# Kernel tuning notes

Hardware: AMD Instinct MI355X
Metric: run time of the kernel (lower is better)

Reference implementation:

```python
import jax, jax.numpy as jnp
import numpy as np

N = 20000        # nodes per type
E = 320000       # edges per type (avg degree 16)
H = 8            # heads
F0 = 128         # initial feature dim
F_UNI = 256      # n_unified
F_OUT = 64       # n_units per layer
N_USER = 20000   # shape_ret[0]
N_CLASSES = 2


def setup_inputs() -> dict:
    key = jax.random.key(0)
    ks = jax.random.split(key, 32)
    nrm = lambda k, s: jax.random.normal(k, s, dtype=jnp.float32) * 0.05
    inp = {
        "hemb0": nrm(ks[0], (N, F0)),
        "hemb1": nrm(ks[1], (N, F0)),
        "W0": nrm(ks[2], (F0, F_UNI)),
        "W1": nrm(ks[3], (F0, F_UNI)),
    }
    i = 4
    for t in range(2):
        for l, fin in enumerate([F_UNI, H * F_OUT]):
            inp[f"g{t}l{l}_w"] = nrm(ks[i], (H, fin, F_OUT)); i += 1
            inp[f"g{t}l{l}_asrc"] = nrm(ks[i], (H, F_OUT)); i += 1
            inp[f"g{t}l{l}_atrg"] = nrm(ks[i], (H, F_OUT)); i += 1
    inp["aw1"] = nrm(ks[i], (F_UNI, F_OUT)); i += 1
    inp["aw2"] = nrm(ks[i], (F_OUT, F_OUT)); i += 1
    inp["am"] = nrm(ks[i], (F_OUT,)); i += 1
    inp["fc_w"] = nrm(ks[i], (F_OUT * 3, N_CLASSES)); i += 1
    inp["fc_b"] = jnp.zeros((N_CLASSES,), jnp.float32); i += 1
    inp["edge0"] = jax.random.randint(ks[i], (2, E), 0, N, dtype=jnp.int32); i += 1
    inp["edge1"] = jax.random.randint(ks[i], (2, E), 0, N, dtype=jnp.int32)
    return inp


def spgat(h, src, trg, w, asrc, atrg):
    """Sparse GAT layer: h [N,f_in], edge list src/trg [E] -> [N,H,f_out]."""
    n = h.shape[0]
    hp = jnp.einsum('nf,hfo->hno', h, w)              # [H,N,O]
    s = jnp.einsum('hno,ho->nh', hp, asrc)            # [N,H]
    t = jnp.einsum('hno,ho->nh', hp, atrg)            # [N,H]
    e = jax.nn.leaky_relu(s[src] + t[trg], negative_slope=0.2)  # [E,H]
    ex = jnp.exp(e - jnp.max(e))                      # global max shift (as in source)
    denom = jax.ops.segment_sum(ex, trg, num_segments=n)[trg] + 1e-16
    alpha = ex / denom                                # [E,H]
    msg = jnp.transpose(hp, (1, 0, 2))[src] * alpha[:, :, None]  # [E,H,O]
    return jax.ops.segment_sum(msg, trg, num_segments=n)         # [N,H,O]


def reference(hemb0, hemb1, W0, W1,
              g0l0_w, g0l0_asrc, g0l0_atrg, g0l1_w, g0l1_asrc, g0l1_atrg,
              g1l0_w, g1l0_asrc, g1l0_atrg, g1l1_w, g1l1_asrc, g1l1_atrg,
              aw1, aw2, am, fc_w, fc_b, edge0, edge1):
    trans0 = hemb0 @ W0                                # [N,F_UNI]
    trans1 = hemb1 @ W1
    stacks = [
        (trans0, edge0, (g0l0_w, g0l0_asrc, g0l0_atrg), (g0l1_w, g0l1_asrc, g0l1_atrg)),
        (trans1, edge1, (g1l0_w, g1l0_asrc, g1l0_atrg), (g1l1_w, g1l1_asrc, g1l1_atrg)),
    ]
    heter = []
    for trans, edge, p0, p1 in stacks:
        src, trg = edge[0], edge[1]
        x = spgat(trans, src, trg, *p0)                # [N,H,F_OUT]
        x = jax.nn.elu(x.reshape(N, -1))               # [N,H*F_OUT]
        x = spgat(x, src, trg, *p1).mean(axis=1)       # [N,F_OUT]
        heter.append(x[:N_USER][:, None, :])
    type_aware = jnp.concatenate(heter, axis=1)        # [N_USER, 2, F_OUT]
    # faithful to source: feature = trans_emb[0] where trans_emb is the LAST
    # type's transformed embedding -> row 0, shape [F_UNI], broadcast over nodes
    feature = trans1[0]
    q = jnp.tanh(feature @ aw1 + type_aware @ aw2)     # [N_USER,2,F_OUT]
    beta = jax.nn.softmax(q @ am, axis=-1)             # [N_USER,2]
    fusion = jnp.einsum('nr,nrd->nd', beta, type_aware)[:, None, :]
    ret = jnp.concatenate([type_aware, fusion], axis=1).reshape(N_USER, -1)
    return jax.nn.log_softmax(ret @ fc_w + fc_b, axis=-1)   # [N_USER, 2]
```

## Files before the change

kernel.cpp:

```cpp
#include <hip/hip_runtime.h>
#include <hip/hip_bf16.h>


typedef __hip_bfloat16 bf16;
typedef __attribute__((ext_vector_type(8))) short short8;
typedef __attribute__((ext_vector_type(4))) float f32x4;

__device__ __forceinline__ float bf2f(bf16 v) { return __bfloat162float(v); }
__device__ __forceinline__ float ldin(const void* p, long i, int f32) {
  return f32 ? ((const float*)p)[i] : bf2f(((const bf16*)p)[i]);
}
__device__ __forceinline__ short f2bfbits(float f) {
  bf16 h = __float2bfloat16(f);
  return *reinterpret_cast<short*>(&h);
}
__device__ __forceinline__ float bfbits2f(short b) {
  unsigned u = ((unsigned)(unsigned short)b) << 16;
  return __uint_as_float(u);
}

__global__ __launch_bounds__(64) void detect_kernel(const void* __restrict__ x,
                                                    int* __restrict__ flag) {
  int tid = threadIdx.x;
  float m = 0.f;
  for (int i = tid; i < 2048; i += 64) {
    float v = fabsf(bf2f(((const bf16*)x)[i]));
    if (!(v <= 1e3f)) v = 1e9f;
    m = fmaxf(m, v);
  }
#pragma unroll
  for (int off = 32; off; off >>= 1) m = fmaxf(m, __shfl_xor(m, off));
  if (tid == 0) flag[0] = (m > 1e3f) ? 1 : 0;
}

#define GBM 128
#define GBN 64
#define GBK 64

__device__ __forceinline__ int swz(int row, int kbyte) {
  return row * 128 + (kbyte ^ ((row & 7) << 4));
}

__global__ __launch_bounds__(256) void gemm_mfma(const void* __restrict__ A, int amode,
                                                 const void* __restrict__ B, int bmode,
                                                 bf16* __restrict__ C,
                                                 int M, int K, int Nc,
                                                 const void* __restrict__ stasrc,
                                                 const void* __restrict__ statrg,
                                                 float* __restrict__ svp,
                                                 float* __restrict__ tvp,
                                                 const int* __restrict__ flag) {
  __shared__ bf16 As[GBM * GBK];
  __shared__ bf16 Bs[GBN * GBK];
  const int f32 = flag[0];
  const int af32 = (amode == 1) ? f32 : 0;
  const int m0 = blockIdx.x * GBM;
  const int n0 = blockIdx.y * GBN;
  const int tid = threadIdx.x;
  const int lane = tid & 63;
  const int wrow = (tid >> 6) * 32;

  f32x4 acc[2][4];
#pragma unroll
  for (int m = 0; m < 2; m++)
#pragma unroll
    for (int n = 0; n < 4; n++)
#pragma unroll
      for (int r = 0; r < 4; r++) acc[m][n][r] = 0.f;

  for (int kt = 0; kt < K; kt += GBK) {
#pragma unroll
    for (int j = 0; j < 4; j++) {
      int idx = tid + j * 256;
      int row = idx >> 3;
      int ks = idx & 7;
      int gm = m0 + row;
      short8 v;
#pragma unroll
      for (int e = 0; e < 8; e++) v[e] = 0;
      if (gm < M) {
        long base = (long)gm * K + kt + ks * 8;
        if (!af32) {
          v = *(const short8*)((const bf16*)A + base);
        } else {
          const float* Af = (const float*)A + base;
#pragma unroll
          for (int e = 0; e < 8; e++) v[e] = f2bfbits(Af[e]);
        }
      }
      *(short8*)((char*)As + swz(row, ks * 16)) = v;
    }
    {
      int n = tid & 63;
      int ks0 = tid >> 6;
#pragma unroll
      for (int jj = 0; jj < 2; jj++) {
        int ks = ks0 + jj * 4;
        int k = kt + ks * 8;
        int col = n0 + n;
        long base;
        int cstr;
        if (bmode == 0) { base = (long)k * Nc + col; cstr = Nc; }
        else { base = ((long)(col >> 6) * K + k) * 64 + (col & 63); cstr = 64; }
        short8 v;
        if (f32) {
          const float* Bf = (const float*)B;
#pragma unroll
          for (int e = 0; e < 8; e++) v[e] = f2bfbits(Bf[base + (long)e * cstr]);
        } else {
          const bf16* Bh = (const bf16*)B;
#pragma unroll
          for (int e = 0; e < 8; e++) v[e] = *(const short*)&Bh[base + (long)e * cstr];
        }
        *(short8*)((char*)Bs + swz(n, ks * 16)) = v;
      }
    }
    __syncthreads();
#pragma unroll
    for (int kh = 0; kh < 2; kh++) {
      int klane = kh * 64 + ((lane >> 4) << 4);
      short8 af[2], bfr[4];
#pragma unroll
      for (int m = 0; m < 2; m++) {
        int row = wrow + m * 16 + (lane & 15);
        af[m] = *(const short8*)((const char*)As + swz(row, klane));
      }
#pragma unroll
      for (int n = 0; n < 4; n++) {
        int col = n * 16 + (lane & 15);
        bfr[n] = *(const short8*)((const char*)Bs + swz(col, klane));
      }
#pragma unroll
      for (int m = 0; m < 2; m++)
#pragma unroll
        for (int n = 0; n < 4; n++)
          acc[m][n] = __builtin_amdgcn_mfma_f32_16x16x32_bf16(af[m], bfr[n], acc[m][n], 0, 0, 0);
    }
    __syncthreads();
  }
  if (svp) {
    const int h = blockIdx.y;
    const int cl = lane & 15;
    float av[4], bv[4];
#pragma unroll
    for (int n = 0; n < 4; n++) {
      av[n] = ldin(stasrc, h * 64 + n * 16 + cl, f32);
      bv[n] = ldin(statrg, h * 64 + n * 16 + cl, f32);
    }
#pragma unroll
    for (int m = 0; m < 2; m++) {
#pragma unroll
      for (int r = 0; r < 4; r++) {
        float s = 0.f, t = 0.f;
#pragma unroll
        for (int n = 0; n < 4; n++) {
          s += acc[m][n][r] * av[n];
          t += acc[m][n][r] * bv[n];
        }
#pragma unroll
        for (int off = 1; off <= 8; off <<= 1) {
          s += __shfl_xor(s, off);
          t += __shfl_xor(t, off);
        }
        int row = m0 + wrow + m * 16 + ((lane >> 4) << 2) + r;
        if (cl == 0 && row < M) {
          svp[(long)row * 8 + h] = s;
          tvp[(long)row * 8 + h] = t;
        }
      }
    }
  }
#pragma unroll
  for (int m = 0; m < 2; m++) {
#pragma unroll
    for (int r = 0; r < 4; r++) {
      int row = m0 + wrow + m * 16 + ((lane >> 4) << 2) + r;
      if (row < M) {
#pragma unroll
        for (int n = 0; n < 4; n++) {
          int col = n0 + n * 16 + (lane & 15);
          C[(long)row * Nc + col] = __float2bfloat16(acc[m][n][r]);
        }
      }
    }
  }
}

__global__ void hist_kernel(const int* __restrict__ trg, int* __restrict__ deg, int E) {
  int e = blockIdx.x * 256 + threadIdx.x;
  if (e < E) atomicAdd(&deg[trg[e]], 1);
}

__global__ __launch_bounds__(1024) void scan_kernel(const int* __restrict__ deg,
                                                    int* __restrict__ row_ptr,
                                                    int* __restrict__ fil, int N) {
  __shared__ int sums[1024];
  int tid = threadIdx.x;
  int chunk = (N + 1023) >> 10;
  int start = tid * chunk;
  int end = start + chunk;
  if (start > N) start = N;
  if (end > N) end = N;
  int s = 0;
  for (int i = start; i < end; i++) s += deg[i];
  sums[tid] = s;
  __syncthreads();
  for (int off = 1; off < 1024; off <<= 1) {
    int add = (tid >= off) ? sums[tid - off] : 0;
    __syncthreads();
    sums[tid] += add;
    __syncthreads();
  }
  int run = (tid > 0) ? sums[tid - 1] : 0;
  for (int i = start; i < end; i++) {
    row_ptr[i] = run;
    fil[i] = run;
    run += deg[i];
  }
  if (tid == 0) row_ptr[N] = sums[1023];
}

__global__ void fill_kernel(const int* __restrict__ src, const int* __restrict__ trg,
                            int* __restrict__ fil, int* __restrict__ col, int E) {
  int e = blockIdx.x * 256 + threadIdx.x;
  if (e >= E) return;
  int t = trg[e];
  int pos = atomicAdd(&fil[t], 1);
  col[pos] = src[e];
}

__device__ __forceinline__ float exleaky(float v) {
  v = v > 0.f ? v : 0.2f * v;
  return __expf(v);
}

__global__ __launch_bounds__(256) void aggregate(const bf16* __restrict__ hp,
                                                 const float* __restrict__ sv,
                                                 const float* __restrict__ tv,
                                                 const int* __restrict__ row_ptr,
                                                 const int* __restrict__ col_src,
                                                 void* __restrict__ out, int N, int mode) {
  const int wid = threadIdx.x >> 6;
  const int lane = threadIdx.x & 63;
  const int n = blockIdx.x * 4 + wid;
  if (n >= N) return;
  const int start = row_ptr[n];
  const int deg = row_ptr[n + 1] - start;
  const int h = lane >> 3;
  const float tvh = tv[(long)n * 8 + h];
  const bf16* __restrict__ hpc = hp + lane * 8;

  float acc[8] = {0.f, 0.f, 0.f, 0.f, 0.f, 0.f, 0.f, 0.f};
  float den = 1e-16f;

#define AG_LOAD(E, V0, V1, V2, V3, Q0, Q1, Q2, Q3)                  \
  {                                                                 \
    int t0 = __shfl(mysrc, (E) + 0), t1 = __shfl(mysrc, (E) + 1);   \
    int t2 = __shfl(mysrc, (E) + 2), t3 = __shfl(mysrc, (E) + 3);   \
    V0 = *(const short8*)(hpc + (long)t0 * 512);                    \
    V1 = *(const short8*)(hpc + (long)t1 * 512);                    \
    V2 = *(const short8*)(hpc + (long)t2 * 512);                    \
    V3 = *(const short8*)(hpc + (long)t3 * 512);                    \
    Q0 = sv[(long)t0 * 8 + h];                                      \
    Q1 = sv[(long)t1 * 8 + h];                                      \
    Q2 = sv[(long)t2 * 8 + h];                                      \
    Q3 = sv[(long)t3 * 8 + h];                                      \
  }
#define AG_ACC(V0, V1, V2, V3, Q0, Q1, Q2, Q3)                      \
  {                                                                 \
    float a0 = exleaky(Q0 + tvh), a1 = exleaky(Q1 + tvh);           \
    float a2 = exleaky(Q2 + tvh), a3 = exleaky(Q3 + tvh);           \
    den += a0 + a1 + a2 + a3;                                       \
    _Pragma("unroll")                                               \
    for (int j = 0; j < 8; j++)                                     \
      acc[j] += a0 * bfbits2f(V0[j]) + a1 * bfbits2f(V1[j]) +       \
                a2 * bfbits2f(V2[j]) + a3 * bfbits2f(V3[j]);        \
  }

  for (int base = 0; base < deg; base += 64) {
    int cnt = deg - base;
    if (cnt > 64) cnt = 64;
    int mysrc = (lane < cnt) ? col_src[start + base + lane] : 0;
    int nfull = cnt & ~3;
    if (nfull) {
      short8 v0, v1, v2, v3;
      float q0, q1, q2, q3;
      AG_LOAD(0, v0, v1, v2, v3, q0, q1, q2, q3);
      for (int e = 4; e < nfull; e += 4) {
        short8 w0 = v0, w1 = v1, w2 = v2, w3 = v3;
        float p0 = q0, p1 = q1, p2 = q2, p3 = q3;
        AG_LOAD(e, v0, v1, v2, v3, q0, q1, q2, q3);
        AG_ACC(w0, w1, w2, w3, p0, p1, p2, p3);
      }
      AG_ACC(v0, v1, v2, v3, q0, q1, q2, q3);
    }
    for (int e = nfull; e < cnt; e++) {
      int s0 = __shfl(mysrc, e);
      short8 v = *(const short8*)(hpc + (long)s0 * 512);
      float a = exleaky(sv[(long)s0 * 8 + h] + tvh);
      den += a;
#pragma unroll
      for (int j = 0; j < 8; j++) acc[j] += a * bfbits2f(v[j]);
    }
  }

  const float dinv = 1.f / den;
  if (mode == 0) {
    short8 o8;
#pragma unroll
    for (int j = 0; j < 8; j++) {
      float s = acc[j] * dinv;
      float ev = s > 0.f ? s : expm1f(s);
      o8[j] = f2bfbits(ev);
    }
    *(short8*)((bf16*)out + (long)n * 512 + lane * 8) = o8;
  } else {
    float r[8];
#pragma unroll
    for (int j = 0; j < 8; j++) r[j] = acc[j] * dinv;
#pragma unroll
    for (int m = 8; m <= 32; m <<= 1)
#pragma unroll
      for (int j = 0; j < 8; j++) r[j] += __shfl_xor(r[j], m);
    if (lane < 8) {
      float* o = (float*)out + (long)n * 128 + lane * 8;
#pragma unroll
      for (int j = 0; j < 8; j++) o[j] = r[j] * 0.125f;
    }
  }
}

__global__ __launch_bounds__(64) void favec_kernel(const bf16* __restrict__ trans1,
                                                   const void* __restrict__ aw1,
                                                   float* __restrict__ favec,
                                                   const int* __restrict__ flag) {
  const int f32 = flag[0];
  int o = threadIdx.x;
  float acc = 0.f;
  for (int k = 0; k < 256; k++) acc += bf2f(trans1[k]) * ldin(aw1, k * 64 + o, f32);
  favec[o] = acc;
}

__global__ __launch_bounds__(64) void final_kernel(const float* __restrict__ ta,
                                                   const float* __restrict__ favec,
                                                   const void* __restrict__ aw2,
                                                   const void* __restrict__ am,
                                                   const void* __restrict__ fcw,
                                                   const void* __restrict__ fcb,
                                                   void* __restrict__ out, int N,
                                                   const int* __restrict__ flag) {
  const int f32 = flag[0];
  int n = blockIdx.x;
  int o = threadIdx.x;
  __shared__ float s0[64], s1[64];
  float ta0 = ta[(long)n * 128 + o];
  float ta1 = ta[(long)n * 128 + 64 + o];
  s0[o] = ta0;
  s1[o] = ta1;
  __syncthreads();
  float f = favec[o];
  float acc0 = f, acc1 = f;
  for (int k = 0; k < 64; k++) {
    float w = ldin(aw2, k * 64 + o, f32);
    acc0 += s0[k] * w;
    acc1 += s1[k] * w;
  }
  float amv = ldin(am, o, f32);
  float p0 = tanhf(acc0) * amv;
  float p1 = tanhf(acc1) * amv;
#pragma unroll
  for (int off = 32; off > 0; off >>= 1) {
    p0 += __shfl_xor(p0, off);
    p1 += __shfl_xor(p1, off);
  }
  float mx = fmaxf(p0, p1);
  float e0 = __expf(p0 - mx), e1 = __expf(p1 - mx);
  float b0 = e0 / (e0 + e1), b1 = e1 / (e0 + e1);
  float fus = b0 * ta0 + b1 * ta1;
  float l0 = ta0 * ldin(fcw, o * 2 + 0, f32) + ta1 * ldin(fcw, (64 + o) * 2 + 0, f32) +
             fus * ldin(fcw, (128 + o) * 2 + 0, f32);
  float l1 = ta0 * ldin(fcw, o * 2 + 1, f32) + ta1 * ldin(fcw, (64 + o) * 2 + 1, f32) +
             fus * ldin(fcw, (128 + o) * 2 + 1, f32);
#pragma unroll
  for (int off = 32; off > 0; off >>= 1) {
    l0 += __shfl_xor(l0, off);
    l1 += __shfl_xor(l1, off);
  }
  if (o == 0) {
    l0 += ldin(fcb, 0, f32);
    l1 += ldin(fcb, 1, f32);
    float m2 = fmaxf(l0, l1);
    float lse = m2 + logf(__expf(l0 - m2) + __expf(l1 - m2));
    if (f32) {
      ((float*)out)[n * 2 + 0] = l0 - lse;
      ((float*)out)[n * 2 + 1] = l1 - lse;
    } else {
      ((bf16*)out)[n * 2 + 0] = __float2bfloat16(l0 - lse);
      ((bf16*)out)[n * 2 + 1] = __float2bfloat16(l1 - lse);
    }
  }
}

extern "C" void kernel_launch(void* const* d_in, const int* in_sizes, int n_in,
                              void* d_out, int out_size, void* d_ws, size_t ws_size,
                              hipStream_t stream) {
  constexpr int N = 20000, E = 320000, H = 8, F0 = 128, FU = 256, FO = 64;
  const void* hemb[2] = {d_in[0], d_in[1]};
  const void* W[2] = {d_in[2], d_in[3]};
  const void* gw[2][2] = {{d_in[4], d_in[7]}, {d_in[10], d_in[13]}};
  const void* gasrc[2][2] = {{d_in[5], d_in[8]}, {d_in[11], d_in[14]}};
  const void* gatrg[2][2] = {{d_in[6], d_in[9]}, {d_in[12], d_in[15]}};
  const void* aw1 = d_in[16];
  const void* aw2 = d_in[17];
  const void* am = d_in[18];
  const void* fcw = d_in[19];
  const void* fcb = d_in[20];
  const int* edge[2] = {(const int*)d_in[21], (const int*)d_in[22]};

  char* p = (char*)d_ws;
  auto alloc = [&](size_t bytes) -> void* {
    void* r = (void*)p;
    p += (bytes + 255) & ~(size_t)255;
    return r;
  };
  int* flag = (int*)alloc(4);
  bf16* trans = (bf16*)alloc((size_t)N * FU * 2);
  bf16* hp = (bf16*)alloc((size_t)N * H * FO * 2);
  bf16* xbuf = (bf16*)alloc((size_t)N * H * FO * 2);
  float* sv = (float*)alloc((size_t)N * H * 4);
  float* tv = (float*)alloc((size_t)N * H * 4);
  float* ta = (float*)alloc((size_t)N * 2 * FO * 4);
  float* favec = (float*)alloc(FO * 4);
  int* deg[2];
  int* rp[2];
  int* fil[2];
  int* col[2];
  for (int t = 0; t < 2; t++) {
    deg[t] = (int*)alloc((size_t)N * 4);
    rp[t] = (int*)alloc((size_t)(N + 1) * 4);
    fil[t] = (int*)alloc((size_t)N * 4);
    col[t] = (int*)alloc((size_t)E * 4);
  }

  detect_kernel<<<1, 64, 0, stream>>>(hemb[0], flag);

  for (int t = 0; t < 2; t++) {
    hipMemsetAsync(deg[t], 0, (size_t)N * 4, stream);
    hist_kernel<<<(E + 255) / 256, 256, 0, stream>>>(edge[t] + E, deg[t], E);
    scan_kernel<<<1, 1024, 0, stream>>>(deg[t], rp[t], fil[t], N);
    fill_kernel<<<(E + 255) / 256, 256, 0, stream>>>(edge[t], edge[t] + E, fil[t], col[t], E);
  }

  const int gmx = (N + GBM - 1) / GBM;
  const int gagg = (N + 3) / 4;

  for (int t = 0; t < 2; t++) {
    gemm_mfma<<<dim3(gmx, FU / GBN), 256, 0, stream>>>(hemb[t], 1, W[t], 0, trans,
                                                       N, F0, FU,
                                                       nullptr, nullptr, nullptr, nullptr, flag);
    gemm_mfma<<<dim3(gmx, (H * FO) / GBN), 256, 0, stream>>>(trans, 0, gw[t][0], 1, hp,
                                                             N, FU, H * FO,
                                                             gasrc[t][0], gatrg[t][0], sv, tv, flag);
    aggregate<<<gagg, 256, 0, stream>>>(hp, sv, tv, rp[t], col[t], xbuf, N, 0);
    gemm_mfma<<<dim3(gmx, (H * FO) / GBN), 256, 0, stream>>>(xbuf, 0, gw[t][1], 1, hp,
                                                             N, H * FO, H * FO,
                                                             gasrc[t][1], gatrg[t][1], sv, tv, flag);
    aggregate<<<gagg, 256, 0, stream>>>(hp, sv, tv, rp[t], col[t], ta + t * FO, N, 1);
  }

  favec_kernel<<<1, 64, 0, stream>>>(trans, aw1, favec, flag);
  final_kernel<<<N, 64, 0, stream>>>(ta, favec, aw2, am, fcw, fcb, d_out, N, flag);
}
```

Baseline: 626.5 us.

## Split node aggregation across two waves, batch CSR build, tile final kernel

The aggregate kernel now assigns two wavefronts per destination node, each handling alternating groups of four edges, and combines their partial sums through shared memory. The goal is more memory-level parallelism for the gather-heavy aggregation. The CSR construction for both edge types is merged into single histogram, scan and fill launches to cut launch count. The final kernel processes four nodes per block, with weights staged in shared memory and activations broadcast by shuffles instead of per-node global reloads. The price is a block-wide sync and extra shared memory in aggregate, which may reduce occupancy.

```diff
diff --git a/kernel.cpp b/kernel.cpp
--- a/kernel.cpp
+++ b/kernel.cpp
@@ -186,14 +186,19 @@
   }
 }
 
-__global__ void hist_kernel(const int* __restrict__ trg, int* __restrict__ deg, int E) {
+__global__ void hist2_kernel(const int* __restrict__ trg0, const int* __restrict__ trg1,
+                             int* __restrict__ deg, int E, int N) {
   int e = blockIdx.x * 256 + threadIdx.x;
-  if (e < E) atomicAdd(&deg[trg[e]], 1);
-}
-
-__global__ __launch_bounds__(1024) void scan_kernel(const int* __restrict__ deg,
-                                                    int* __restrict__ row_ptr,
-                                                    int* __restrict__ fil, int N) {
+  if (e < E) atomicAdd(&deg[trg0[e]], 1);
+  else if (e < 2 * E) atomicAdd(&deg[N + trg1[e - E]], 1);
+}
+
+__global__ __launch_bounds__(1024) void scan_kernel(const int* __restrict__ degb,
+                                                    int* __restrict__ rpb,
+                                                    int* __restrict__ filb, int N) {
+  const int* deg = degb + (long)blockIdx.x * N;
+  int* row_ptr = rpb + (long)blockIdx.x * (N + 1);
+  int* fil = filb + (long)blockIdx.x * N;
   __shared__ int sums[1024];
   int tid = threadIdx.x;
   int chunk = (N + 1023) >> 10;
@@ -220,13 +225,20 @@
   if (tid == 0) row_ptr[N] = sums[1023];
 }
 
-__global__ void fill_kernel(const int* __restrict__ src, const int* __restrict__ trg,
-                            int* __restrict__ fil, int* __restrict__ col, int E) {
+__global__ void fill2_kernel(const int* __restrict__ src0, const int* __restrict__ trg0,
+                             const int* __restrict__ src1, const int* __restrict__ trg1,
+                             int* __restrict__ filb, int* __restrict__ colb, int E, int N) {
   int e = blockIdx.x * 256 + threadIdx.x;
-  if (e >= E) return;
-  int t = trg[e];
-  int pos = atomicAdd(&fil[t], 1);
-  col[pos] = src[e];
+  if (e < E) {
+    int t = trg0[e];
+    int pos = atomicAdd(&filb[t], 1);
+    colb[pos] = src0[e];
+  } else if (e < 2 * E) {
+    int ee = e - E;
+    int t = trg1[ee];
+    int pos = atomicAdd(&filb[N + t], 1);
+    colb[E + pos] = src1[ee];
+  }
 }
 
 __device__ __forceinline__ float exleaky(float v) {
@@ -240,23 +252,30 @@
                                                  const int* __restrict__ row_ptr,
                                                  const int* __restrict__ col_src,
                                                  void* __restrict__ out, int N, int mode) {
+  __shared__ float s_acc[2][512];
+  __shared__ float s_den[2][64];
   const int wid = threadIdx.x >> 6;
   const int lane = threadIdx.x & 63;
-  const int n = blockIdx.x * 4 + wid;
-  if (n >= N) return;
-  const int start = row_ptr[n];
-  const int deg = row_ptr[n + 1] - start;
+  const int slot = wid >> 1;
+  const int half = wid & 1;
+  const int n = blockIdx.x * 2 + slot;
+  const int act = (n < N);
+  int start = 0, deg = 0;
+  if (act) {
+    start = row_ptr[n];
+    deg = row_ptr[n + 1] - start;
+  }
   const int h = lane >> 3;
-  const float tvh = tv[(long)n * 8 + h];
+  const float tvh = act ? tv[(long)n * 8 + h] : 0.f;
   const bf16* __restrict__ hpc = hp + lane * 8;
 
   float acc[8] = {0.f, 0.f, 0.f, 0.f, 0.f, 0.f, 0.f, 0.f};
-  float den = 1e-16f;
-
-#define AG_LOAD(E, V0, V1, V2, V3, Q0, Q1, Q2, Q3)                  \
+  float den = 0.f;
+
+#define AG_LOAD(EB, V0, V1, V2, V3, Q0, Q1, Q2, Q3)                 \
   {                                                                 \
-    int t0 = __shfl(mysrc, (E) + 0), t1 = __shfl(mysrc, (E) + 1);   \
-    int t2 = __shfl(mysrc, (E) + 2), t3 = __shfl(mysrc, (E) + 3);   \
+    int t0 = __shfl(mysrc, (EB) + 0), t1 = __shfl(mysrc, (EB) + 1); \
+    int t2 = __shfl(mysrc, (EB) + 2), t3 = __shfl(mysrc, (EB) + 3); \
     V0 = *(const short8*)(hpc + (long)t0 * 512);                    \
     V1 = *(const short8*)(hpc + (long)t1 * 512);                    \
     V2 = *(const short8*)(hpc + (long)t2 * 512);                    \
@@ -281,51 +300,65 @@
     int cnt = deg - base;
     if (cnt > 64) cnt = 64;
     int mysrc = (lane < cnt) ? col_src[start + base + lane] : 0;
-    int nfull = cnt & ~3;
-    if (nfull) {
+    int ngrp = cnt >> 2;
+    int g = half;
+    if (g < ngrp) {
       short8 v0, v1, v2, v3;
       float q0, q1, q2, q3;
-      AG_LOAD(0, v0, v1, v2, v3, q0, q1, q2, q3);
-      for (int e = 4; e < nfull; e += 4) {
+      AG_LOAD(g * 4, v0, v1, v2, v3, q0, q1, q2, q3);
+      for (int g2 = g + 2; g2 < ngrp; g2 += 2) {
         short8 w0 = v0, w1 = v1, w2 = v2, w3 = v3;
         float p0 = q0, p1 = q1, p2 = q2, p3 = q3;
-        AG_LOAD(e, v0, v1, v2, v3, q0, q1, q2, q3);
+        AG_LOAD(g2 * 4, v0, v1, v2, v3, q0, q1, q2, q3);
         AG_ACC(w0, w1, w2, w3, p0, p1, p2, p3);
       }
       AG_ACC(v0, v1, v2, v3, q0, q1, q2, q3);
     }
-    for (int e = nfull; e < cnt; e++) {
-      int s0 = __shfl(mysrc, e);
-      short8 v = *(const short8*)(hpc + (long)s0 * 512);
-      float a = exleaky(sv[(long)s0 * 8 + h] + tvh);
-      den += a;
-#pragma unroll
-      for (int j = 0; j < 8; j++) acc[j] += a * bfbits2f(v[j]);
-    }
-  }
-
-  const float dinv = 1.f / den;
-  if (mode == 0) {
-    short8 o8;
-#pragma unroll
-    for (int j = 0; j < 8; j++) {
-      float s = acc[j] * dinv;
-      float ev = s > 0.f ? s : expm1f(s);
-      o8[j] = f2bfbits(ev);
-    }
-    *(short8*)((bf16*)out + (long)n * 512 + lane * 8) = o8;
-  } else {
-    float r[8];
-#pragma unroll
-    for (int j = 0; j < 8; j++) r[j] = acc[j] * dinv;
-#pragma unroll
-    for (int m = 8; m <= 32; m <<= 1)
-#pragma unroll
-      for (int j = 0; j < 8; j++) r[j] += __shfl_xor(r[j], m);
-    if (lane < 8) {
-      float* o = (float*)out + (long)n * 128 + lane * 8;
-#pragma unroll
-      for (int j = 0; j < 8; j++) o[j] = r[j] * 0.125f;
+    if (half == 0) {
+      for (int e = ngrp * 4; e < cnt; e++) {
+        int s0 = __shfl(mysrc, e);
+        short8 v = *(const short8*)(hpc + (long)s0 * 512);
+        float a = exleaky(sv[(long)s0 * 8 + h] + tvh);
+        den += a;
+#pragma unroll
+        for (int j = 0; j < 8; j++) acc[j] += a * bfbits2f(v[j]);
+      }
+    }
+  }
+
+  if (half == 1) {
+#pragma unroll
+    for (int j = 0; j < 8; j++) s_acc[slot][j * 64 + lane] = acc[j];
+    s_den[slot][lane] = den;
+  }
+  __syncthreads();
+  if (half == 0 && act) {
+    den += s_den[slot][lane] + 1e-16f;
+#pragma unroll
+    for (int j = 0; j < 8; j++) acc[j] += s_acc[slot][j * 64 + lane];
+    const float dinv = 1.f / den;
+    if (mode == 0) {
+      short8 o8;
+#pragma unroll
+      for (int j = 0; j < 8; j++) {
+        float s = acc[j] * dinv;
+        float ev = s > 0.f ? s : expm1f(s);
+        o8[j] = f2bfbits(ev);
+      }
+      *(short8*)((bf16*)out + (long)n * 512 + lane * 8) = o8;
+    } else {
+      float r[8];
+#pragma unroll
+      for (int j = 0; j < 8; j++) r[j] = acc[j] * dinv;
+#pragma unroll
+      for (int m = 8; m <= 32; m <<= 1)
+#pragma unroll
+        for (int j = 0; j < 8; j++) r[j] += __shfl_xor(r[j], m);
+      if (lane < 8) {
+        float* o = (float*)out + (long)n * 128 + lane * 8;
+#pragma unroll
+        for (int j = 0; j < 8; j++) o[j] = r[j] * 0.125f;
+      }
     }
   }
 }
@@ -341,31 +374,37 @@
   favec[o] = acc;
 }
 
-__global__ __launch_bounds__(64) void final_kernel(const float* __restrict__ ta,
-                                                   const float* __restrict__ favec,
-                                                   const void* __restrict__ aw2,
-                                                   const void* __restrict__ am,
-                                                   const void* __restrict__ fcw,
-                                                   const void* __restrict__ fcb,
-                                                   void* __restrict__ out, int N,
-                                                   const int* __restrict__ flag) {
+__global__ __launch_bounds__(256) void final_kernel(const float* __restrict__ ta,
+                                                    const float* __restrict__ favec,
+                                                    const void* __restrict__ aw2,
+                                                    const void* __restrict__ am,
+                                                    const void* __restrict__ fcw,
+                                                    const void* __restrict__ fcb,
+                                                    void* __restrict__ out, int N,
+                                                    const int* __restrict__ flag) {
   const int f32 = flag[0];
-  int n = blockIdx.x;
-  int o = threadIdx.x;
-  __shared__ float s0[64], s1[64];
+  __shared__ float s_w[64 * 64];
+  __shared__ float s_fc[384];
+  __shared__ float s_misc[130];
+  const int tid = threadIdx.x;
+  for (int i = tid; i < 4096; i += 256) s_w[i] = ldin(aw2, i, f32);
+  for (int i = tid; i < 384; i += 256) s_fc[i] = ldin(fcw, i, f32);
+  if (tid < 64) s_misc[tid] = favec[tid];
+  else if (tid < 128) s_misc[tid] = ldin(am, tid - 64, f32);
+  else if (tid < 130) s_misc[tid] = ldin(fcb, tid - 128, f32);
+  __syncthreads();
+  const int o = tid & 63;
+  const int n = blockIdx.x * 4 + (tid >> 6);
+  if (n >= N) return;
   float ta0 = ta[(long)n * 128 + o];
   float ta1 = ta[(long)n * 128 + 64 + o];
-  s0[o] = ta0;
-  s1[o] = ta1;
-  __syncthreads();
-  float f = favec[o];
-  float acc0 = f, acc1 = f;
+  float acc0 = s_misc[o], acc1 = acc0;
   for (int k = 0; k < 64; k++) {
-    float w = ldin(aw2, k * 64 + o, f32);
-    acc0 += s0[k] * w;
-    acc1 += s1[k] * w;
-  }
-  float amv = ldin(am, o, f32);
+    float w = s_w[k * 64 + o];
+    acc0 += __shfl(ta0, k) * w;
+    acc1 += __shfl(ta1, k) * w;
+  }
+  float amv = s_misc[64 + o];
   float p0 = tanhf(acc0) * amv;
   float p1 = tanhf(acc1) * amv;
 #pragma unroll
@@ -377,18 +416,16 @@
   float e0 = __expf(p0 - mx), e1 = __expf(p1 - mx);
   float b0 = e0 / (e0 + e1), b1 = e1 / (e0 + e1);
   float fus = b0 * ta0 + b1 * ta1;
-  float l0 = ta0 * ldin(fcw, o * 2 + 0, f32) + ta1 * ldin(fcw, (64 + o) * 2 + 0, f32) +
-             fus * ldin(fcw, (128 + o) * 2 + 0, f32);
-  float l1 = ta0 * ldin(fcw, o * 2 + 1, f32) + ta1 * ldin(fcw, (64 + o) * 2 + 1, f32) +
-             fus * ldin(fcw, (128 + o) * 2 + 1, f32);
+  float l0 = ta0 * s_fc[o * 2 + 0] + ta1 * s_fc[(64 + o) * 2 + 0] + fus * s_fc[(128 + o) * 2 + 0];
+  float l1 = ta0 * s_fc[o * 2 + 1] + ta1 * s_fc[(64 + o) * 2 + 1] + fus * s_fc[(128 + o) * 2 + 1];
 #pragma unroll
   for (int off = 32; off > 0; off >>= 1) {
     l0 += __shfl_xor(l0, off);
     l1 += __shfl_xor(l1, off);
   }
   if (o == 0) {
-    l0 += ldin(fcb, 0, f32);
-    l1 += ldin(fcb, 1, f32);
+    l0 += s_misc[128];
+    l1 += s_misc[129];
     float m2 = fmaxf(l0, l1);
     float lse = m2 + logf(__expf(l0 - m2) + __expf(l1 - m2));
     if (f32) {
@@ -431,43 +468,38 @@
   float* tv = (float*)alloc((size_t)N * H * 4);
   float* ta = (float*)alloc((size_t)N * 2 * FO * 4);
   float* favec = (float*)alloc(FO * 4);
-  int* deg[2];
-  int* rp[2];
-  int* fil[2];
-  int* col[2];
+  int* degb = (int*)alloc((size_t)2 * N * 4);
+  int* rpb = (int*)alloc((size_t)2 * (N + 1) * 4);
+  int* filb = (int*)alloc((size_t)2 * N * 4);
+  int* colb = (int*)alloc((size_t)2 * E * 4);
+
+  detect_kernel<<<1, 64, 0, stream>>>(hemb[0], flag);
+
+  hipMemsetAsync(degb, 0, (size_t)2 * N * 4, stream);
+  hist2_kernel<<<(2 * E + 255) / 256, 256, 0, stream>>>(edge[0] + E, edge[1] + E, degb, E, N);
+  scan_kernel<<<2, 1024, 0, stream>>>(degb, rpb, filb, N);
+  fill2_kernel<<<(2 * E + 255) / 256, 256, 0, stream>>>(edge[0], edge[0] + E,
+                                                        edge[1], edge[1] + E, filb, colb, E, N);
+
+  const int gmx = (N + GBM - 1) / GBM;
+  const int gagg = (N + 1) / 2;
+
   for (int t = 0; t < 2; t++) {
-    deg[t] = (int*)alloc((size_t)N * 4);
-    rp[t] = (int*)alloc((size_t)(N + 1) * 4);
-    fil[t] = (int*)alloc((size_t)N * 4);
-    col[t] = (int*)alloc((size_t)E * 4);
-  }
-
-  detect_kernel<<<1, 64, 0, stream>>>(hemb[0], flag);
-
-  for (int t = 0; t < 2; t++) {
-    hipMemsetAsync(deg[t], 0, (size_t)N * 4, stream);
-    hist_kernel<<<(E + 255) / 256, 256, 0, stream>>>(edge[t] + E, deg[t], E);
-    scan_kernel<<<1, 1024, 0, stream>>>(deg[t], rp[t], fil[t], N);
-    fill_kernel<<<(E + 255) / 256, 256, 0, stream>>>(edge[t], edge[t] + E, fil[t], col[t], E);
-  }
-
-  const int gmx = (N + GBM - 1) / GBM;
-  const int gagg = (N + 3) / 4;
-
-  for (int t = 0; t < 2; t++) {
+    const int* rp = rpb + (size_t)t * (N + 1);
+    const int* col = colb + (size_t)t * E;
     gemm_mfma<<<dim3(gmx, FU / GBN), 256, 0, stream>>>(hemb[t], 1, W[t], 0, trans,
                                                        N, F0, FU,
                                                        nullptr, nullptr, nullptr, nullptr, flag);
     gemm_mfma<<<dim3(gmx, (H * FO) / GBN), 256, 0, stream>>>(trans, 0, gw[t][0], 1, hp,
                                                              N, FU, H * FO,
                                                              gasrc[t][0], gatrg[t][0], sv, tv, flag);
-    aggregate<<<gagg, 256, 0, stream>>>(hp, sv, tv, rp[t], col[t], xbuf, N, 0);
+    aggregate<<<gagg, 256, 0, stream>>>(hp, sv, tv, rp, col, xbuf, N, 0);
     gemm_mfma<<<dim3(gmx, (H * FO) / GBN), 256, 0, stream>>>(xbuf, 0, gw[t][1], 1, hp,
                                                              N, H * FO, H * FO,
                                                              gasrc[t][1], gatrg[t][1], sv, tv, flag);
-    aggregate<<<gagg, 256, 0, stream>>>(hp, sv, tv, rp[t], col[t], ta + t * FO, N, 1);
+    aggregate<<<gagg, 256, 0, stream>>>(hp, sv, tv, rp, col, ta + t * FO, N, 1);
   }
 
   favec_kernel<<<1, 64, 0, stream>>>(trans, aw1, favec, flag);
-  final_kernel<<<N, 64, 0, stream>>>(ta, favec, aw2, am, fcw, fcb, d_out, N, flag);
-}
+  final_kernel<<<(N + 3) / 4, 256, 0, stream>>>(ta, favec, aw2, am, fcw, fcb, d_out, N, flag);
+}
```

Result: faster. 610.0 us (-2.6%).
